# Kernel tuning notes

Measured on AMD Instinct MI355X. Metric: run time of the kernel, lower is better.

Reference implementation:

```python
import jax, jax.numpy as jnp
import numpy as np

B, S, D_IN, D_OUT, RANK = 4, 2048, 4096, 4096, 16
ALPHA = 16
SCALING = ALPHA / RANK  # 1.0


def setup_inputs() -> dict:
    key = jax.random.key(0)
    k_x, k_q, k_b, k_a, k_bb = jax.random.split(key, 5)
    x = jax.random.normal(k_x, (B, S, D_IN), dtype=jnp.float32)
    # int4 symmetric quantized weight values in [-8, 7], stored as int32
    qweight = jax.random.randint(k_q, (D_OUT, D_IN), -8, 8, dtype=jnp.int32)
    # per-tensor scale (abs_max / 7 in the original); a plausible small value
    scales = jnp.array([0.01], dtype=jnp.float32)
    bias = jax.random.normal(k_b, (D_OUT,), dtype=jnp.float32) * 0.02
    # LoRA params (acting as "trained" values; original inits A kaiming, B zeros)
    lora_A = jax.random.normal(k_a, (D_IN, RANK), dtype=jnp.float32) * (1.0 / np.sqrt(D_IN))
    lora_B = jax.random.normal(k_bb, (RANK, D_OUT), dtype=jnp.float32) * 0.01
    return {"x": x, "qweight": qweight, "scales": scales, "bias": bias,
            "lora_A": lora_A, "lora_B": lora_B}


def reference(x, qweight, scales, bias, lora_A, lora_B):
    # dequantize: int4 values * scalar scale -> fp32 weight [D_OUT, D_IN]
    w = qweight.astype(jnp.float32) * scales[0]
    # F.linear(x, w, bias): x @ w.T + bias
    out = jnp.einsum('bsd,od->bso', x, w) + bias
    # LoRA low-rank path: (x @ A) @ B * scaling (dropout=0 -> identity)
    lora_out = (x @ lora_A) @ lora_B
    return out + lora_out * SCALING
```

## Files before the change

### kernel.cpp

```cpp
#include <hip/hip_runtime.h>
#include <stdint.h>
#include <math.h>


static constexpr int Mdim = 8192;
static constexpr int Ndim = 4096;
static constexpr int Kdim = 4096;

typedef __bf16 bf16x8 __attribute__((ext_vector_type(8)));
typedef float f32x4 __attribute__((ext_vector_type(4)));
typedef int   i32x4 __attribute__((ext_vector_type(4)));

__device__ __forceinline__ void async_copy16(const void* gptr, void* lptr) {
    auto g = (const __attribute__((address_space(1))) unsigned char*)(uintptr_t)gptr;
    auto l = (__attribute__((address_space(3))) unsigned char*)(uintptr_t)lptr;
    __builtin_amdgcn_global_load_lds(g, l, 16, 0, 0);
}

static constexpr int BLK_W = Ndim * Kdim / (256 * 16);
static constexpr int BLK_X = Mdim;
static constexpr int BLK_BT = Ndim / 256;

__global__ void __launch_bounds__(256) prep_kernel(
        const float* __restrict__ x,
        const int* __restrict__ qw,
        const float* __restrict__ lA,
        const float* __restrict__ lB,
        int8_t* __restrict__ x_i8,
        int8_t* __restrict__ w_i8,
        int8_t* __restrict__ a_i8t,
        __bf16* __restrict__ Blbt,
        float* __restrict__ row_scale,
        float* __restrict__ a_scale_g,
        float* __restrict__ xabf) {
    __shared__ float red[8];
    int b = blockIdx.x;
    const int tid = threadIdx.x;

    if (b == 0) {
        float am = 0.f;
        const float4* ap = (const float4*)lA + tid * 64;
        for (int i = 0; i < 64; ++i) {
            float4 v = ap[i];
            am = fmaxf(am, fmaxf(fmaxf(fabsf(v.x), fabsf(v.y)),
                                 fmaxf(fabsf(v.z), fabsf(v.w))));
        }
        for (int off = 32; off; off >>= 1) am = fmaxf(am, __shfl_xor(am, off));
        if ((tid & 63) == 0) red[tid >> 6] = am;
        __syncthreads();
        if (tid == 0) {
            float m = fmaxf(fmaxf(red[0], red[1]), fmaxf(red[2], red[3]));
            red[4] = m;
            a_scale_g[0] = m > 0.f ? m / 127.f : 0.f;
        }
        __syncthreads();
        float amax = red[4];
        float inv = amax > 0.f ? 127.f / amax : 0.f;
        int k0 = tid * 16;
#pragma unroll
        for (int r = 0; r < 16; ++r) {
            int8_t o[16];
#pragma unroll
            for (int kk = 0; kk < 16; ++kk) {
                float v = lA[(size_t)(k0 + kk) * 16 + r];
                o[kk] = (int8_t)(int)rintf(v * inv);
            }
            *(i32x4*)(a_i8t + (size_t)r * Kdim + k0) = *(i32x4*)o;
        }
        return;
    }
    b -= 1;

    if (b < BLK_W) {
        size_t idx = ((size_t)b * 256 + tid) * 16;
        const int4* q = (const int4*)(qw + idx);
        int4 q0 = q[0], q1 = q[1], q2 = q[2], q3 = q[3];
        int8_t o[16] = {(int8_t)q0.x, (int8_t)q0.y, (int8_t)q0.z, (int8_t)q0.w,
                        (int8_t)q1.x, (int8_t)q1.y, (int8_t)q1.z, (int8_t)q1.w,
                        (int8_t)q2.x, (int8_t)q2.y, (int8_t)q2.z, (int8_t)q2.w,
                        (int8_t)q3.x, (int8_t)q3.y, (int8_t)q3.z, (int8_t)q3.w};
        *(i32x4*)(w_i8 + idx) = *(i32x4*)o;
        return;
    }
    b -= BLK_W;

    if (b < BLK_X) {
        const int row = b;
        const float4* xp = (const float4*)(x + (size_t)row * Kdim) + tid * 4;
        float4 v0 = xp[0], v1 = xp[1], v2 = xp[2], v3 = xp[3];
        float am = 0.f;
        am = fmaxf(am, fmaxf(fmaxf(fabsf(v0.x), fabsf(v0.y)), fmaxf(fabsf(v0.z), fabsf(v0.w))));
        am = fmaxf(am, fmaxf(fmaxf(fabsf(v1.x), fabsf(v1.y)), fmaxf(fabsf(v1.z), fabsf(v1.w))));
        am = fmaxf(am, fmaxf(fmaxf(fabsf(v2.x), fabsf(v2.y)), fmaxf(fabsf(v2.z), fabsf(v2.w))));
        am = fmaxf(am, fmaxf(fmaxf(fabsf(v3.x), fabsf(v3.y)), fmaxf(fabsf(v3.z), fabsf(v3.w))));
        for (int off = 32; off; off >>= 1) am = fmaxf(am, __shfl_xor(am, off));
        if ((tid & 63) == 0) red[tid >> 6] = am;
        __syncthreads();
        if (tid == 0) {
            float m = fmaxf(fmaxf(red[0], red[1]), fmaxf(red[2], red[3]));
            red[4] = m;
            row_scale[row] = m > 0.f ? m / 127.f : 0.f;
        }
        __syncthreads();
        float amax = red[4];
        float inv = amax > 0.f ? 127.f / amax : 0.f;
        float vv[16] = {v0.x, v0.y, v0.z, v0.w, v1.x, v1.y, v1.z, v1.w,
                        v2.x, v2.y, v2.z, v2.w, v3.x, v3.y, v3.z, v3.w};
        int8_t o[16];
#pragma unroll
        for (int i = 0; i < 16; ++i) o[i] = (int8_t)(int)rintf(vv[i] * inv);
        *(i32x4*)(x_i8 + (size_t)row * Kdim + tid * 16) = *(i32x4*)o;
        return;
    }
    b -= BLK_X;

    {
        int c = b * 256 + tid;
        __bf16 tmp[16];
#pragma unroll
        for (int r = 0; r < 16; ++r) tmp[r] = (__bf16)lB[(size_t)r * Ndim + c];
        *(bf16x8*)(Blbt + (size_t)c * 16) = *(bf16x8*)tmp;
        *(bf16x8*)(Blbt + (size_t)c * 16 + 8) = *(bf16x8*)(tmp + 8);
        f32x4 z = {0.f, 0.f, 0.f, 0.f};
        f32x4* zp = (f32x4*)(xabf + (size_t)(b * 256 + tid) * 32);
#pragma unroll
        for (int i = 0; i < 8; ++i) zp[i] = z;
    }
}

__global__ void __launch_bounds__(256) xa_kernel(
        const int8_t* __restrict__ x_i8,
        const int8_t* __restrict__ a_i8t,
        const float* __restrict__ row_scale,
        const float* __restrict__ a_scale_g,
        float* __restrict__ xabf) {
    __shared__ __align__(16) char sX[2][4096];
    __shared__ __align__(16) char sAq[2][1024];
    const int tid = threadIdx.x, wave = tid >> 6, lane = tid & 63;
    const int quad = lane >> 4, l16 = lane & 15;
    const int bm = blockIdx.x >> 2;
    const int kc = blockIdx.x & 3;
    const int kbeg = kc * (Kdim / 4);

    const size_t xoff = (size_t)(bm * 64 + (tid & 63)) * Kdim + (tid >> 6) * 16;
    const size_t aoff = (size_t)(tid & 15) * Kdim + (tid >> 4) * 16;

    i32x4 acc = {0, 0, 0, 0};
    async_copy16(x_i8 + xoff + kbeg, sX[0] + tid * 16);
    if (tid < 64) async_copy16(a_i8t + aoff + kbeg, sAq[0] + tid * 16);
    __syncthreads();
    int cur = 0;
    const int rdA = (quad * 64 + wave * 16 + l16) * 16;
    const int rdB = (quad * 16 + l16) * 16;
#pragma unroll 1
    for (int t = 0; t < 16; ++t) {
        if (t < 15) {
            async_copy16(x_i8 + xoff + kbeg + (t + 1) * 64, sX[cur ^ 1] + tid * 16);
            if (tid < 64)
                async_copy16(a_i8t + aoff + kbeg + (t + 1) * 64, sAq[cur ^ 1] + tid * 16);
        }
        i32x4 af = *(const i32x4*)(sX[cur] + rdA);
        i32x4 bf = *(const i32x4*)(sAq[cur] + rdB);
        acc = __builtin_amdgcn_mfma_i32_16x16x64_i8(af, bf, acc, 0, 0, 0);
        __syncthreads();
        cur ^= 1;
    }
    const float asc = a_scale_g[0];
    const int rl = wave * 16 + quad * 4;
#pragma unroll
    for (int r = 0; r < 4; ++r) {
        int grow = bm * 64 + rl + r;
        float v = (float)acc[r] * row_scale[grow] * asc;
        atomicAdd(xabf + (size_t)grow * 16 + l16, v);
    }
}

__global__ void __launch_bounds__(256) gemm_kernel(
        const int8_t* __restrict__ Xq,
        const int8_t* __restrict__ Wq,
        const float* __restrict__ scales,
        const float* __restrict__ bias,
        const float* __restrict__ row_scale,
        const float* __restrict__ xabf,
        const __bf16* __restrict__ Blbt,
        float* __restrict__ out) {
    __shared__ __align__(16) char smem[32768];

    const int tid = threadIdx.x, wave = tid >> 6, lane = tid & 63;
    const int wm = wave >> 1, wn = wave & 1;
    const int quad = lane >> 4, l16 = lane & 15;

    const int bid = blockIdx.y * gridDim.x + blockIdx.x;
    const int xcd = bid & 7;
    const int local = bid >> 3;
    const int bm = (xcd >> 1) * 16 + (local >> 4);
    const int bn = (xcd & 1) * 16 + (local & 15);

    const int srow = tid & 127;
    const int sq = tid >> 7;
    const size_t a_off0 = (size_t)(bm * 128 + srow) * Kdim + sq * 16;
    const size_t a_off1 = a_off0 + 32;
    const size_t b_off0 = (size_t)(bn * 128 + srow) * Kdim + sq * 16;
    const size_t b_off1 = b_off0 + 32;
    const int dst0 = tid * 16, dst1 = 4096 + tid * 16;

    const int aoffL = quad * 2048 + (wm * 64 + l16) * 16;
    const int boffL = quad * 2048 + (wn * 64 + l16) * 16;

    i32x4 acc[4][4];
#pragma unroll
    for (int i = 0; i < 4; ++i)
#pragma unroll
        for (int j = 0; j < 4; ++j) acc[i][j] = i32x4{0, 0, 0, 0};

    auto stage = [&](int k0, char* PA, char* PB) {
        async_copy16(Xq + a_off0 + k0, PA + dst0);
        async_copy16(Xq + a_off1 + k0, PA + dst1);
        async_copy16(Wq + b_off0 + k0, PB + dst0);
        async_copy16(Wq + b_off1 + k0, PB + dst1);
    };
    auto compute = [&](const char* PA, const char* PB) {
        i32x4 aF[4], bF[4];
#pragma unroll
        for (int i = 0; i < 4; ++i) aF[i] = *(const i32x4*)(PA + aoffL + i * 256);
#pragma unroll
        for (int j = 0; j < 4; ++j) bF[j] = *(const i32x4*)(PB + boffL + j * 256);
#pragma unroll
        for (int i = 0; i < 4; ++i)
#pragma unroll
            for (int j = 0; j < 4; ++j)
                acc[i][j] = __builtin_amdgcn_mfma_i32_16x16x64_i8(aF[i], bF[j], acc[i][j], 0, 0, 0);
    };

    stage(0, smem, smem + 8192);
    __syncthreads();
    int cur = 0;
#pragma unroll 1
    for (int t = 0; t < 63; ++t) {
        char* nxt = smem + ((cur ^ 1) << 14);
        stage((t + 1) * 64, nxt, nxt + 8192);
        char* c = smem + (cur << 14);
        compute(c, c + 8192);
        __syncthreads();
        cur ^= 1;
    }
    {
        char* c = smem + (cur << 14);
        compute(c, c + 8192);
    }

    const float wsc = scales[0];
    float bj4[4];
#pragma unroll
    for (int j = 0; j < 4; ++j) bj4[j] = bias[bn * 128 + wn * 64 + j * 16 + l16];

    __syncthreads();
    async_copy16((const char*)xabf + (size_t)bm * 128 * 64 + tid * 16, smem + tid * 16);
    async_copy16((const char*)xabf + (size_t)bm * 128 * 64 + 4096 + tid * 16,
                 smem + 4096 + tid * 16);
    async_copy16((const char*)(Blbt + (size_t)bn * 128 * 16) + tid * 16,
                 smem + 8192 + tid * 16);
    if (tid < 32)
        async_copy16((const char*)(row_scale + bm * 128) + tid * 16,
                     smem + 12288 + tid * 16);
    __syncthreads();

    const float*  sXAf = (const float*)smem;
    const __bf16* sBL  = (const __bf16*)(smem + 8192);
    const float*  sRS  = (const float*)(smem + 12288);

    bf16x8 zf;
#pragma unroll
    for (int k = 0; k < 8; ++k) zf[k] = (__bf16)0.f;

    bf16x8 aF2[4], bF2[4];
#pragma unroll
    for (int i = 0; i < 4; ++i) {
        if (quad < 2) {
            const float* p = sXAf + (wm * 64 + i * 16 + l16) * 16 + quad * 8;
            f32x4 u0 = *(const f32x4*)p;
            f32x4 u1 = *(const f32x4*)(p + 4);
            bf16x8 t;
            t[0] = (__bf16)u0[0]; t[1] = (__bf16)u0[1];
            t[2] = (__bf16)u0[2]; t[3] = (__bf16)u0[3];
            t[4] = (__bf16)u1[0]; t[5] = (__bf16)u1[1];
            t[6] = (__bf16)u1[2]; t[7] = (__bf16)u1[3];
            aF2[i] = t;
        } else {
            aF2[i] = zf;
        }
    }
#pragma unroll
    for (int j = 0; j < 4; ++j) {
        if (quad < 2) bF2[j] = *(const bf16x8*)(sBL + (wn * 64 + j * 16 + l16) * 16 + quad * 8);
        else          bF2[j] = zf;
    }

    f32x4 lacc[4][4];
#pragma unroll
    for (int j = 0; j < 4; ++j)
#pragma unroll
        for (int i = 0; i < 4; ++i)
            lacc[i][j] = f32x4{bj4[j], bj4[j], bj4[j], bj4[j]};

#pragma unroll
    for (int i = 0; i < 4; ++i)
#pragma unroll
        for (int j = 0; j < 4; ++j)
            lacc[i][j] = __builtin_amdgcn_mfma_f32_16x16x32_bf16(aF2[i], bF2[j], lacc[i][j], 0, 0, 0);

    const int col0 = bn * 128 + wn * 64 + l16;
    const int rl0 = wm * 64 + quad * 4;
#pragma unroll
    for (int j = 0; j < 4; ++j) {
        const int col = col0 + j * 16;
#pragma unroll
        for (int i = 0; i < 4; ++i) {
            const int lr = rl0 + i * 16;
#pragma unroll
            for (int r = 0; r < 4; ++r) {
                float sx = sRS[lr + r] * wsc;
                out[(size_t)(bm * 128 + lr + r) * Ndim + col] =
                    (float)acc[i][j][r] * sx + lacc[i][j][r];
            }
        }
    }
}

extern "C" void kernel_launch(void* const* d_in, const int* in_sizes, int n_in,
                              void* d_out, int out_size, void* d_ws, size_t ws_size,
                              hipStream_t stream) {
    const float* x      = (const float*)d_in[0];
    const int*   qw     = (const int*)d_in[1];
    const float* scales = (const float*)d_in[2];
    const float* bias   = (const float*)d_in[3];
    const float* lA     = (const float*)d_in[4];
    const float* lB     = (const float*)d_in[5];
    float* out = (float*)d_out;

    char* ws = (char*)d_ws;
    int8_t* x_i8     = (int8_t*)ws;
    int8_t* w_i8     = (int8_t*)(ws + 33554432);
    int8_t* a_i8t    = (int8_t*)(ws + 50331648);
    float*  xabf     = (float*)(ws + 50397184);
    __bf16* Blbt     = (__bf16*)(ws + 50921472);
    float*  row_scale = (float*)(ws + 51052544);
    float*  a_scale_g = (float*)(ws + 51085312);

    const int prep_blocks = 1 + BLK_W + BLK_X + BLK_BT;
    prep_kernel<<<prep_blocks, 256, 0, stream>>>(
        x, qw, lA, lB, x_i8, w_i8, a_i8t, Blbt, row_scale, a_scale_g, xabf);
    xa_kernel<<<512, 256, 0, stream>>>(x_i8, a_i8t, row_scale, a_scale_g, xabf);
    dim3 grid(Ndim / 128, Mdim / 128);
    gemm_kernel<<<grid, 256, 0, stream>>>(x_i8, w_i8, scales, bias, row_scale,
                                          xabf, Blbt, out);
}
```

Measured before the change: 553.2 us.

## Replace syncthreads with partial vmcnt waits and raise priority around MFMAs

```diff
diff --git a/kernel.cpp b/kernel.cpp
--- a/kernel.cpp
+++ b/kernel.cpp
@@ -16,6 +16,9 @@
     auto l = (__attribute__((address_space(3))) unsigned char*)(uintptr_t)lptr;
     __builtin_amdgcn_global_load_lds(g, l, 16, 0, 0);
 }
+
+#define ASM_VMCNT4 asm volatile("s_waitcnt vmcnt(4)" ::: "memory")
+#define ASM_VMCNT0 asm volatile("s_waitcnt vmcnt(0)" ::: "memory")
 
 static constexpr int BLK_W = Ndim * Kdim / (256 * 16);
 static constexpr int BLK_X = Mdim;
@@ -213,6 +216,11 @@
 #pragma unroll
         for (int j = 0; j < 4; ++j) acc[i][j] = i32x4{0, 0, 0, 0};
 
+    char* const sA0 = smem;
+    char* const sB0 = smem + 8192;
+    char* const sA1 = smem + 16384;
+    char* const sB1 = smem + 24576;
+
     auto stage = [&](int k0, char* PA, char* PB) {
         async_copy16(Xq + a_off0 + k0, PA + dst0);
         async_copy16(Xq + a_off1 + k0, PA + dst1);
@@ -225,29 +233,38 @@
         for (int i = 0; i < 4; ++i) aF[i] = *(const i32x4*)(PA + aoffL + i * 256);
 #pragma unroll
         for (int j = 0; j < 4; ++j) bF[j] = *(const i32x4*)(PB + boffL + j * 256);
+        __builtin_amdgcn_s_setprio(1);
 #pragma unroll
         for (int i = 0; i < 4; ++i)
 #pragma unroll
             for (int j = 0; j < 4; ++j)
                 acc[i][j] = __builtin_amdgcn_mfma_i32_16x16x64_i8(aF[i], bF[j], acc[i][j], 0, 0, 0);
+        __builtin_amdgcn_s_setprio(0);
     };
 
-    stage(0, smem, smem + 8192);
-    __syncthreads();
-    int cur = 0;
+    stage(0, sA0, sB0);
 #pragma unroll 1
-    for (int t = 0; t < 63; ++t) {
-        char* nxt = smem + ((cur ^ 1) << 14);
-        stage((t + 1) * 64, nxt, nxt + 8192);
-        char* c = smem + (cur << 14);
-        compute(c, c + 8192);
-        __syncthreads();
-        cur ^= 1;
-    }
-    {
-        char* c = smem + (cur << 14);
-        compute(c, c + 8192);
-    }
+    for (int t = 0; t < 31; ++t) {
+        const int k = t * 128;
+        stage(k + 64, sA1, sB1);
+        ASM_VMCNT4;
+        __builtin_amdgcn_s_barrier();
+        compute(sA0, sB0);
+        __builtin_amdgcn_s_barrier();
+        stage(k + 128, sA0, sB0);
+        ASM_VMCNT4;
+        __builtin_amdgcn_s_barrier();
+        compute(sA1, sB1);
+        __builtin_amdgcn_s_barrier();
+    }
+    stage(63 * 64, sA1, sB1);
+    ASM_VMCNT4;
+    __builtin_amdgcn_s_barrier();
+    compute(sA0, sB0);
+    __builtin_amdgcn_s_barrier();
+    ASM_VMCNT0;
+    __builtin_amdgcn_s_barrier();
+    compute(sA1, sB1);
 
     const float wsc = scales[0];
     float bj4[4];
```

Measured after the change: 554.2 us. No clear change (+0.2%).
